# Kernel optimization log

Measured on AMD Instinct MI355X. Metric: run time of the kernel, lower is better.

Reference implementation:

```python
import jax, jax.numpy as jnp
import numpy as np

EPS = 1e-8  # torch F.cosine_similarity default eps


def setup_inputs() -> dict:
    key = jax.random.key(0)
    ks = jax.random.split(key, 8)
    B, N, D, H = 2, 256, 256, 8
    LEN = 2 * D + 4  # flag == 1
    query = jax.random.normal(ks[0], (B, N, N, D), dtype=jnp.float32)
    k_in = jax.random.normal(ks[1], (B, N, N, D), dtype=jnp.float32)
    s_query = jax.random.uniform(ks[2], (B, N, N, 2), dtype=jnp.float32)
    s_key = jax.random.uniform(ks[3], (B, N, N, 2), dtype=jnp.float32)
    roi_mask = jnp.ones((B, N, N), dtype=jnp.float32)
    # nn.Linear(LEN, H) params
    bound = 1.0 / np.sqrt(LEN)
    W = jax.random.uniform(ks[4], (H, LEN), minval=-bound, maxval=bound, dtype=jnp.float32)
    b_lin = jax.random.uniform(ks[5], (H,), minval=-bound, maxval=bound, dtype=jnp.float32)
    return {"query": query, "key": k_in, "s_query": s_query, "s_key": s_key,
            "roi_mask": roi_mask, "W": W, "b_lin": b_lin, "node_num": 32}


def reference(query, key, s_query, s_key, roi_mask, W, b_lin, node_num):
    B, N, _, D = query.shape
    # spatial feature for flag==1: simple concat
    spat = jnp.concatenate([s_query, s_key], axis=3)          # (B,N,N,4)
    ft = jnp.concatenate([query, key, spat], axis=3)          # (B,N,N,2D+4)
    attn1 = jax.nn.sigmoid(jnp.einsum('bqkc,hc->bqkh', ft, W) + b_lin)  # (B,N,N,H)

    # cosine-similarity scores over channel dim, then relu (Attention_4)
    qn = jnp.maximum(jnp.sqrt(jnp.sum(query * query, axis=3)), EPS)
    kn = jnp.maximum(jnp.sqrt(jnp.sum(key * key, axis=3)), EPS)
    scores = jnp.sum(query * key, axis=3) / (qn * kn)         # (B,N,N)
    attn = jax.nn.relu(scores)

    # torch: values, idces = topk(attn(B,N,N,1), node_num, dim=2);
    #        atten_mask[:, :, idces, :] = 1.0
    # Fancy indexing with the full idces tensor sets dim-2 position p to 1
    # for ALL (b, row) whenever p appears ANYWHERE in idces -> a global
    # indicator vector along dim 2.
    _, idces = jax.lax.top_k(attn, node_num)                  # (B,N,node_num)
    ind = jnp.zeros((N,), dtype=attn1.dtype).at[idces.reshape(-1)].set(1.0)

    out = attn1 * roi_mask[:, :, :, None] * ind[None, None, :, None]
    return out
```

## Files before the change

kernel.cpp:

```cpp
#include <hip/hip_runtime.h>

#define NPAIR 131072
#define NDIM  256
#define NH    8
#define NN    256
#define NROWS 512
#define LEN   516
#define EPSV  1e-8f

__device__ __forceinline__ float dot4(float4 a, float4 b) {
    return fmaf(a.x, b.x, fmaf(a.y, b.y, fmaf(a.z, b.z, a.w * b.w)));
}

#define DPP_ADD(x, ctrl)                                                        \
    x += __int_as_float(__builtin_amdgcn_update_dpp(                            \
        0, __float_as_int(x), (ctrl), 0xf, 0xf, false))

__device__ __forceinline__ float wave_sum(float x) {
    DPP_ADD(x, 0x111);
    DPP_ADD(x, 0x112);
    DPP_ADD(x, 0x114);
    DPP_ADD(x, 0x118);
    DPP_ADD(x, 0x142);
    DPP_ADD(x, 0x143);
    return __int_as_float(
        __builtin_amdgcn_readlane(__float_as_int(x), 63));
}

__global__ __launch_bounds__(256) void fused_main(
    const float* __restrict__ Q, const float* __restrict__ K,
    const float* __restrict__ SQ, const float* __restrict__ SK,
    const float* __restrict__ ROI, const float* __restrict__ W,
    const float* __restrict__ Bb, float* __restrict__ out,
    float* __restrict__ scores)
{
    const int lane = threadIdx.x & 63;
    const int h = lane & 7;
    const int nwaves = (gridDim.x * blockDim.x) >> 6;
    const int wave = (blockIdx.x * blockDim.x + threadIdx.x) >> 6;

    float4 wq[NH], wk[NH];
#pragma unroll
    for (int i = 0; i < NH; i++) {
        wq[i] = *(const float4*)(W + i * LEN + lane * 4);
        wk[i] = *(const float4*)(W + i * LEN + 256 + lane * 4);
    }
    const float4 wt = *(const float4*)(W + h * LEN + 512);
    const float bh = Bb[h];

    for (int p0 = wave; p0 < NPAIR; p0 += nwaves) {
        const int p = __builtin_amdgcn_readfirstlane(p0);
        const float4 qv = *(const float4*)(Q + (size_t)p * NDIM + lane * 4);
        const float4 kv = *(const float4*)(K + (size_t)p * NDIM + lane * 4);

        float aqq = dot4(qv, qv);
        float akk = dot4(kv, kv);
        float aqk = dot4(qv, kv);
        float sh[2 * NH];
#pragma unroll
        for (int i = 0; i < NH; i++) {
            sh[i]      = dot4(qv, wq[i]);
            sh[NH + i] = dot4(kv, wk[i]);
        }

        const float qq = wave_sum(aqq);
        const float kk = wave_sum(akk);
        const float qk = wave_sum(aqk);

        float x = 0.0f;
#pragma unroll
        for (int i = 0; i < NH; i++) {
            const float si = wave_sum(sh[i]) + wave_sum(sh[NH + i]);
            x = (h == i) ? si : x;
        }

        float qn = fmaxf(sqrtf(qq), EPSV);
        float kn = fmaxf(sqrtf(kk), EPSV);
        float sc = fmaxf(qk / (qn * kn), 0.0f);
        if (lane == 0) scores[p] = sc;

        const float sq0 = SQ[2 * p], sq1 = SQ[2 * p + 1];
        const float sk0 = SK[2 * p], sk1 = SK[2 * p + 1];
        x += sq0 * wt.x + sq1 * wt.y + sk0 * wt.z + sk1 * wt.w + bh;
        float y = 1.0f / (1.0f + __expf(-x));
        y *= ROI[p];
        if (lane < NH) out[(size_t)p * NH + lane] = y;
    }
}

__global__ void zero_ind(float* __restrict__ ind) {
    ind[threadIdx.x] = 0.0f;
}

__global__ __launch_bounds__(64) void topk_kernel(
    const float* __restrict__ scores, float* __restrict__ ind,
    const int* __restrict__ node_num)
{
    const int row = blockIdx.x;
    const int lane = threadIdx.x;
    const float4 v4 = *(const float4*)(scores + row * NN + lane * 4);
    float v[4] = {v4.x, v4.y, v4.z, v4.w};

    int Kk = node_num[0];
    if (Kk > NN) Kk = NN;
    for (int t = 0; t < Kk; t++) {
        float mv = v[0];
        int mi = lane * 4;
#pragma unroll
        for (int j = 1; j < 4; j++) {
            if (v[j] > mv) { mv = v[j]; mi = lane * 4 + j; }
        }
        for (int off = 32; off > 0; off >>= 1) {
            const float ov = __shfl_xor(mv, off, 64);
            const int   oi = __shfl_xor(mi, off, 64);
            if (ov > mv || (ov == mv && oi < mi)) { mv = ov; mi = oi; }
        }
        if (lane == 0) ind[mi] = 1.0f;
        if ((mi >> 2) == lane) v[mi & 3] = -1.0f;
    }
}

__global__ __launch_bounds__(256) void apply_ind_kernel(
    float* __restrict__ out, const float* __restrict__ ind)
{
    const int i = blockIdx.x * blockDim.x + threadIdx.x;
    float4 v = ((float4*)out)[i];
    const float m = ind[(i >> 1) & (NN - 1)];
    v.x *= m; v.y *= m; v.z *= m; v.w *= m;
    ((float4*)out)[i] = v;
}

extern "C" void kernel_launch(void* const* d_in, const int* in_sizes, int n_in,
                              void* d_out, int out_size, void* d_ws, size_t ws_size,
                              hipStream_t stream)
{
    const float* Q   = (const float*)d_in[0];
    const float* K   = (const float*)d_in[1];
    const float* SQ  = (const float*)d_in[2];
    const float* SK  = (const float*)d_in[3];
    const float* ROI = (const float*)d_in[4];
    const float* W   = (const float*)d_in[5];
    const float* Bb  = (const float*)d_in[6];
    const int* node_num = (const int*)d_in[7];

    float* out = (float*)d_out;
    float* scores = (float*)d_ws;
    float* ind = scores + NPAIR;

    fused_main<<<1024, 256, 0, stream>>>(Q, K, SQ, SK, ROI, W, Bb, out, scores);
    zero_ind<<<1, 256, 0, stream>>>(ind);
    topk_kernel<<<NROWS, 64, 0, stream>>>(scores, ind, node_num);
    apply_ind_kernel<<<out_size / 4 / 256, 256, 0, stream>>>(out, ind);
}
```

Baseline: 321.1 us.

## Assign one pair per lane via LDS transpose instead of wave-per-pair reductions

The main kernel now maps each of a block's 64 lanes to one (q,k) pair. Q/K chunks are staged through XOR-swizzled LDS tiles, with register prefetch of the next chunk, so every lane accumulates its own dot products serially. This removes the 19 cross-lane DPP reductions per pair and lets each lane write its 8 outputs as two float4 stores. In exchange it adds LDS traffic, block barriers and scalar W loads from cache, and launches 2048 small 64-thread blocks.

```diff
diff --git a/kernel.cpp b/kernel.cpp
--- a/kernel.cpp
+++ b/kernel.cpp
@@ -12,80 +12,101 @@
     return fmaf(a.x, b.x, fmaf(a.y, b.y, fmaf(a.z, b.z, a.w * b.w)));
 }
 
-#define DPP_ADD(x, ctrl)                                                        \
-    x += __int_as_float(__builtin_amdgcn_update_dpp(                            \
-        0, __float_as_int(x), (ctrl), 0xf, 0xf, false))
-
-__device__ __forceinline__ float wave_sum(float x) {
-    DPP_ADD(x, 0x111);
-    DPP_ADD(x, 0x112);
-    DPP_ADD(x, 0x114);
-    DPP_ADD(x, 0x118);
-    DPP_ADD(x, 0x142);
-    DPP_ADD(x, 0x143);
-    return __int_as_float(
-        __builtin_amdgcn_readlane(__float_as_int(x), 63));
-}
-
-__global__ __launch_bounds__(256) void fused_main(
+__global__ __launch_bounds__(64) void fused_main(
     const float* __restrict__ Q, const float* __restrict__ K,
     const float* __restrict__ SQ, const float* __restrict__ SK,
     const float* __restrict__ ROI, const float* __restrict__ W,
     const float* __restrict__ Bb, float* __restrict__ out,
     float* __restrict__ scores)
 {
-    const int lane = threadIdx.x & 63;
-    const int h = lane & 7;
-    const int nwaves = (gridDim.x * blockDim.x) >> 6;
-    const int wave = (blockIdx.x * blockDim.x + threadIdx.x) >> 6;
+    __shared__ float4 ldsQ[512];
+    __shared__ float4 ldsK[512];
 
-    float4 wq[NH], wk[NH];
+    const int lane = threadIdx.x;
+    const int p0 = blockIdx.x * 64;
+    const int rsub = lane >> 3;
+    const int jcol = lane & 7;
+
+    const float4* Q4 = (const float4*)Q;
+    const float4* K4 = (const float4*)K;
+
+    float acc[11];
 #pragma unroll
-    for (int i = 0; i < NH; i++) {
-        wq[i] = *(const float4*)(W + i * LEN + lane * 4);
-        wk[i] = *(const float4*)(W + i * LEN + 256 + lane * 4);
+    for (int i = 0; i < 11; ++i) acc[i] = 0.0f;
+
+    float4 gq[8], gk[8];
+#pragma unroll
+    for (int t = 0; t < 8; ++t) {
+        const int r = rsub + 8 * t;
+        gq[t] = Q4[(size_t)(p0 + r) * 64 + jcol];
+        gk[t] = K4[(size_t)(p0 + r) * 64 + jcol];
     }
-    const float4 wt = *(const float4*)(W + h * LEN + 512);
-    const float bh = Bb[h];
 
-    for (int p0 = wave; p0 < NPAIR; p0 += nwaves) {
-        const int p = __builtin_amdgcn_readfirstlane(p0);
-        const float4 qv = *(const float4*)(Q + (size_t)p * NDIM + lane * 4);
-        const float4 kv = *(const float4*)(K + (size_t)p * NDIM + lane * 4);
+    for (int c = 0; c < 8; ++c) {
+        __syncthreads();
+#pragma unroll
+        for (int t = 0; t < 8; ++t) {
+            const int r = rsub + 8 * t;
+            const int a = r * 8 + (jcol ^ rsub);
+            ldsQ[a] = gq[t];
+            ldsK[a] = gk[t];
+        }
+        if (c < 7) {
+#pragma unroll
+            for (int t = 0; t < 8; ++t) {
+                const int r = rsub + 8 * t;
+                gq[t] = Q4[(size_t)(p0 + r) * 64 + (c + 1) * 8 + jcol];
+                gk[t] = K4[(size_t)(p0 + r) * 64 + (c + 1) * 8 + jcol];
+            }
+        }
+        __syncthreads();
 
-        float aqq = dot4(qv, qv);
-        float akk = dot4(kv, kv);
-        float aqk = dot4(qv, kv);
-        float sh[2 * NH];
+        float4 qc[8], kc[8];
 #pragma unroll
-        for (int i = 0; i < NH; i++) {
-            sh[i]      = dot4(qv, wq[i]);
-            sh[NH + i] = dot4(kv, wk[i]);
+        for (int j = 0; j < 8; ++j) {
+            const int a = lane * 8 + (j ^ (lane & 7));
+            qc[j] = ldsQ[a];
+            kc[j] = ldsK[a];
         }
 
-        const float qq = wave_sum(aqq);
-        const float kk = wave_sum(akk);
-        const float qk = wave_sum(aqk);
+#pragma unroll
+        for (int j = 0; j < 8; ++j) {
+            acc[8]  += dot4(qc[j], kc[j]);
+            acc[9]  += dot4(qc[j], qc[j]);
+            acc[10] += dot4(kc[j], kc[j]);
+        }
+#pragma unroll
+        for (int h = 0; h < NH; ++h) {
+            const float4* wq = (const float4*)(W + h * LEN + c * 32);
+            const float4* wk = (const float4*)(W + h * LEN + 256 + c * 32);
+            float a0 = 0.0f;
+#pragma unroll
+            for (int j = 0; j < 8; ++j) {
+                a0 += dot4(qc[j], wq[j]);
+                a0 += dot4(kc[j], wk[j]);
+            }
+            acc[h] += a0;
+        }
+    }
 
-        float x = 0.0f;
+    const int p = p0 + lane;
+    const float qn = fmaxf(sqrtf(acc[9]),  EPSV);
+    const float kn = fmaxf(sqrtf(acc[10]), EPSV);
+    scores[p] = fmaxf(acc[8] / (qn * kn), 0.0f);
+
+    const float2 sq = ((const float2*)SQ)[p];
+    const float2 sk = ((const float2*)SK)[p];
+    const float roi = ROI[p];
+    float ov[NH];
 #pragma unroll
-        for (int i = 0; i < NH; i++) {
-            const float si = wave_sum(sh[i]) + wave_sum(sh[NH + i]);
-            x = (h == i) ? si : x;
-        }
-
-        float qn = fmaxf(sqrtf(qq), EPSV);
-        float kn = fmaxf(sqrtf(kk), EPSV);
-        float sc = fmaxf(qk / (qn * kn), 0.0f);
-        if (lane == 0) scores[p] = sc;
-
-        const float sq0 = SQ[2 * p], sq1 = SQ[2 * p + 1];
-        const float sk0 = SK[2 * p], sk1 = SK[2 * p + 1];
-        x += sq0 * wt.x + sq1 * wt.y + sk0 * wt.z + sk1 * wt.w + bh;
-        float y = 1.0f / (1.0f + __expf(-x));
-        y *= ROI[p];
-        if (lane < NH) out[(size_t)p * NH + lane] = y;
+    for (int h = 0; h < NH; ++h) {
+        const float4 wt = *(const float4*)(W + h * LEN + 512);
+        float x = acc[h] + sq.x * wt.x + sq.y * wt.y
+                         + sk.x * wt.z + sk.y * wt.w + Bb[h];
+        ov[h] = roi / (1.0f + __expf(-x));
     }
+    ((float4*)out)[(size_t)p * 2]     = make_float4(ov[0], ov[1], ov[2], ov[3]);
+    ((float4*)out)[(size_t)p * 2 + 1] = make_float4(ov[4], ov[5], ov[6], ov[7]);
 }
 
 __global__ void zero_ind(float* __restrict__ ind) {
@@ -147,7 +168,7 @@
     float* scores = (float*)d_ws;
     float* ind = scores + NPAIR;
 
-    fused_main<<<1024, 256, 0, stream>>>(Q, K, SQ, SK, ROI, W, Bb, out, scores);
+    fused_main<<<NPAIR / 64, 64, 0, stream>>>(Q, K, SQ, SK, ROI, W, Bb, out, scores);
     zero_ind<<<1, 256, 0, stream>>>(ind);
     topk_kernel<<<NROWS, 64, 0, stream>>>(scores, ind, node_num);
     apply_ind_kernel<<<out_size / 4 / 256, 256, 0, stream>>>(out, ind);
```

Measured after the change: 382.3 us. +19.1%, slower.
